# Kernel optimization log

Hardware: AMD Instinct MI355X
Metric: run time of the kernel (lower is better)

The kernel has to match this reference:

```python
import jax, jax.numpy as jnp
import numpy as np

B, S, D_MODEL, H, D = 2, 2048, 1024, 16, 64
SCALE = 1.0 / float(np.sqrt(D))


def setup_inputs() -> dict:
    key = jax.random.key(0)
    ks = jax.random.split(key, 5)
    x = jax.random.normal(ks[0], (B, S, D_MODEL), jnp.float32)
    qkv_w = jax.random.normal(ks[1], (3 * H * D, D_MODEL), jnp.float32) * 0.02
    out_w = jax.random.normal(ks[2], (D_MODEL, H * D), jnp.float32) * 0.02
    bias_p = jax.random.uniform(ks[3], (H, 1, 1), jnp.float32) * 2.0  # torch.rand(...)*2
    bias_a = jax.random.uniform(ks[4], (H, 1, 1), jnp.float32)
    # standard geometric RoPE frequencies over d_head//2 = 32 channels
    rope_freqs = 10000.0 ** (-jnp.arange(D // 2, dtype=jnp.float32) / (D // 2))
    return {"x": x, "qkv_w": qkv_w, "out_w": out_w,
            "bias_p": bias_p, "bias_a": bias_a, "rope_freqs": rope_freqs}


def _rope(t, c, s):
    # t: [B,H,S,d]; c,s: [1,1,S,d/2]. Split-half rotation as in apply_rope.
    d2 = t.shape[-1] // 2
    t1, t2 = t[..., :d2], t[..., d2:]
    return jnp.concatenate([t1 * c - t2 * s, t1 * s + t2 * c], axis=-1)


def reference(x, qkv_w, out_w, bias_p, bias_a, rope_freqs):
    Bb, Ss, _ = x.shape
    qkv = (x @ qkv_w.T).reshape(Bb, Ss, 3, H, D)
    q = qkv[:, :, 0].transpose(0, 2, 1, 3)  # [B,H,S,d]
    k = qkv[:, :, 1].transpose(0, 2, 1, 3)
    v = qkv[:, :, 2].transpose(0, 2, 1, 3)
    pos = jnp.arange(Ss, dtype=jnp.float32)
    ang = pos[:, None] * rope_freqs[None, :]                 # [S, d/2]
    c = jnp.cos(ang)[None, None]
    s = jnp.sin(ang)[None, None]
    q = _rope(q, c, s)
    k = _rope(k, c, s)
    scores = jnp.einsum('bhqd,bhkd->bhqk', q, k) * SCALE     # [B,H,S,S]
    p = jnp.maximum(bias_p, 0.01)                            # clamp(min=0.01)
    a = jnp.maximum(bias_a, 0.01)
    dist = jnp.abs(pos[None, :] - pos[:, None])              # [S,S]
    kb = -p * jnp.log1p(a * dist)                            # [H,S,S]
    attn = jax.nn.softmax(scores + kb[None], axis=-1)
    out = jnp.einsum('bhqk,bhkd->bhqd', attn, v)             # [B,H,S,d]
    out = out.transpose(0, 2, 1, 3).reshape(Bb, Ss, H * D)
    return out @ out_w.T
```

## Files before the change

kernel.cpp:

```cpp
#include <hip/hip_runtime.h>
#include <math.h>

#define BATCH  2
#define SEQ    2048
#define DMODEL 1024
#define NH     16
#define HD     64
#define NQKV   3072
#define ROWS   (BATCH*SEQ)
#define QSCALE 0.18033688f

typedef unsigned short u16;
typedef unsigned int   u32;
typedef __bf16 bf16x8 __attribute__((ext_vector_type(8)));
typedef float  f32x4  __attribute__((ext_vector_type(4)));

typedef const __attribute__((address_space(1))) void* gptr_t;
typedef __attribute__((address_space(3))) void* lptr_t;

__device__ __forceinline__ void gload16(lptr_t l, const void* g) {
    __builtin_amdgcn_global_load_lds((gptr_t)g, l, 16, 0, 0);
}

__device__ __forceinline__ u16 f2bf(float f) {
    unsigned int u = __float_as_uint(f);
    u += 0x7FFFu + ((u >> 16) & 1u);
    return (u16)(u >> 16);
}
__device__ __forceinline__ u32 pk2(float lo, float hi) {
#if __has_builtin(__builtin_amdgcn_cvt_pk_bf16_f32)
    typedef __bf16 bf16x2 __attribute__((ext_vector_type(2)));
    union { bf16x2 v; u32 u; } cv;
    cv.v = __builtin_amdgcn_cvt_pk_bf16_f32(lo, hi);
    return cv.u;
#else
    return (u32)f2bf(lo) | ((u32)f2bf(hi) << 16);
#endif
}
__device__ __forceinline__ float fexp2(float x) {
#if __has_builtin(__builtin_amdgcn_exp2f)
    return __builtin_amdgcn_exp2f(x);
#else
    return exp2f(x);
#endif
}

#define NBC ((ROWS*DMODEL + NQKV*DMODEL + DMODEL*DMODEL) / 1024)
__global__ void prep_kernel(const float* __restrict__ a,
                            const float* __restrict__ b,
                            const float* __restrict__ c,
                            u16* __restrict__ oa, u16* __restrict__ ob,
                            u16* __restrict__ oc,
                            const float* __restrict__ freqs, float* __restrict__ cs_tab,
                            const float* __restrict__ bias_p,
                            const float* __restrict__ bias_a,
                            float* __restrict__ wtab)
{
    const int na = ROWS*DMODEL, nb = NQKV*DMODEL;
    int blk = blockIdx.x;
    if (blk < NBC) {
        int i = (blk * 256 + threadIdx.x) * 4;
        const float* s; u16* d; int base;
        if (i < na)           { s = a; d = oa; base = i; }
        else if (i < na + nb) { s = b; d = ob; base = i - na; }
        else                  { s = c; d = oc; base = i - na - nb; }
        float4 v = *(const float4*)(s + base);
        u16 o[4] = { f2bf(v.x), f2bf(v.y), f2bf(v.z), f2bf(v.w) };
        *(uint2*)(d + base) = *(const uint2*)o;
    } else if (blk < NBC + 256) {
        int idx = (blk - NBC) * 256 + threadIdx.x;
        int s = idx >> 5, d = idx & 31;
        float sn, cs;
        sincosf((float)s * freqs[d], &sn, &cs);
        cs_tab[idx * 2]     = cs;
        cs_tab[idx * 2 + 1] = sn;
    } else {
        int idx = (blk - NBC - 256) * 256 + threadIdx.x;
        int h = idx >> 11;
        int d = idx & (SEQ - 1);
        float p = fmaxf(bias_p[h], 0.01f);
        float aa = fmaxf(bias_a[h], 0.01f);
        wtab[idx] = __expf(-p * log1pf(aa * (float)d));
    }
}

__global__ __launch_bounds__(256) void gemm_qkv(
    const u16* __restrict__ A, const u16* __restrict__ B,
    const float* __restrict__ cs_tab,
    u16* __restrict__ Qb, u16* __restrict__ Kb, u16* __restrict__ Vt)
{
    const int K = DMODEL;
    __shared__ __align__(16) u16 As[128][32];
    __shared__ __align__(16) u16 Bs[128][32];
    const int tid  = threadIdx.x;
    const int wave = tid >> 6, lane = tid & 63;
    const int quad = lane >> 4, l16 = lane & 15;
    const int wrow = (wave >> 1) * 64, wcol = (wave & 1) * 64;
    const int bm = blockIdx.x * 128, bn = blockIdx.y * 128;

    const int srow = lane >> 2;
    const int scol = ((lane & 3) ^ (srow & 3)) * 8;
    const int fsw = (quad ^ (l16 & 3)) * 8;

    f32x4 acc[4][4];
#pragma unroll
    for (int i = 0; i < 4; ++i)
#pragma unroll
        for (int j = 0; j < 4; ++j) acc[i][j] = (f32x4){0.f,0.f,0.f,0.f};

    const u16* Ag0 = A + (size_t)(bm + wave*32 + srow)      * K + scol;
    const u16* Ag1 = A + (size_t)(bm + wave*32 + 16 + srow) * K + scol;
    const u16* Bg0 = B + (size_t)(bn + wave*32 + srow)      * K + scol;
    const u16* Bg1 = B + (size_t)(bn + wave*32 + 16 + srow) * K + scol;

    for (int k0 = 0; k0 < K; k0 += 32) {
        __syncthreads();
        gload16((lptr_t)&As[wave*32][0],      Ag0 + k0);
        gload16((lptr_t)&As[wave*32 + 16][0], Ag1 + k0);
        gload16((lptr_t)&Bs[wave*32][0],      Bg0 + k0);
        gload16((lptr_t)&Bs[wave*32 + 16][0], Bg1 + k0);
        __syncthreads();
        bf16x8 af[4], bfr[4];
#pragma unroll
        for (int i = 0; i < 4; ++i)
            af[i] = *(const bf16x8*)&As[wrow + i*16 + l16][fsw];
#pragma unroll
        for (int j = 0; j < 4; ++j)
            bfr[j] = *(const bf16x8*)&Bs[wcol + j*16 + l16][fsw];
#pragma unroll
        for (int i = 0; i < 4; ++i)
#pragma unroll
            for (int j = 0; j < 4; ++j)
                acc[i][j] = __builtin_amdgcn_mfma_f32_16x16x32_bf16(af[i], bfr[j], acc[i][j], 0, 0, 0);
    }

    const int tcol = (bn + wcol) >> 6;
    const int t = tcol >> 4, h = tcol & 15;
    const int bq = bm >> 11;
    const int sb = (bm & (SEQ - 1)) + wrow;
    const size_t hb = (size_t)(bq * NH + h) * SEQ * HD;

    if (t == 2) {
#pragma unroll
        for (int i = 0; i < 4; ++i) {
            const int s = sb + i*16 + quad*4;
#pragma unroll
            for (int j = 0; j < 4; ++j) {
                const int d = j*16 + l16;
                uint2 pv = make_uint2(pk2(acc[i][j][0], acc[i][j][1]),
                                      pk2(acc[i][j][2], acc[i][j][3]));
                *(uint2*)&Vt[hb + (size_t)d * SEQ + s] = pv;
            }
        }
    } else {
        const float sc = (t == 0) ? QSCALE : 1.0f;
        u16* dstb = ((t == 0) ? Qb : Kb) + hb;
#pragma unroll
        for (int i = 0; i < 4; ++i) {
#pragma unroll
            for (int r = 0; r < 4; ++r) {
                const int s = sb + i*16 + quad*4 + r;
                const float2* ct = (const float2*)(cs_tab + ((size_t)s * 32 + l16) * 2);
                float2 cs0 = ct[0];
                float2 cs1 = ct[16];
                float a0 = acc[i][0][r], a1 = acc[i][1][r];
                float a2 = acc[i][2][r], a3 = acc[i][3][r];
                u16* dst = dstb + (size_t)s * HD;
                dst[l16]      = f2bf((a0*cs0.x - a2*cs0.y) * sc);
                dst[16 + l16] = f2bf((a1*cs1.x - a3*cs1.y) * sc);
                dst[32 + l16] = f2bf((a0*cs0.y + a2*cs0.x) * sc);
                dst[48 + l16] = f2bf((a1*cs1.y + a3*cs1.x) * sc);
            }
        }
    }
}

__global__ __launch_bounds__(256) void gemm_out(
    const u16* __restrict__ A, const u16* __restrict__ B,
    float* __restrict__ Cout, int M, int N, int K)
{
    __shared__ __align__(16) u16 As[128][32];
    __shared__ __align__(16) u16 Bs[64][32];
    const int tid  = threadIdx.x;
    const int wave = tid >> 6, lane = tid & 63;
    const int quad = lane >> 4, l16 = lane & 15;
    const int wrow = (wave >> 1) * 64, wcol = (wave & 1) * 32;
    const int bm = blockIdx.x * 128, bn = blockIdx.y * 64;

    const int srow = lane >> 2;
    const int scol = ((lane & 3) ^ (srow & 3)) * 8;
    const int fsw = (quad ^ (l16 & 3)) * 8;

    f32x4 acc[4][2];
#pragma unroll
    for (int i = 0; i < 4; ++i)
#pragma unroll
        for (int j = 0; j < 2; ++j) acc[i][j] = (f32x4){0.f,0.f,0.f,0.f};

    const u16* Ag0 = A + (size_t)(bm + wave*32 + srow)      * K + scol;
    const u16* Ag1 = A + (size_t)(bm + wave*32 + 16 + srow) * K + scol;
    const u16* Bg0 = B + (size_t)(bn + wave*16 + srow)      * K + scol;

    for (int k0 = 0; k0 < K; k0 += 32) {
        __syncthreads();
        gload16((lptr_t)&As[wave*32][0],      Ag0 + k0);
        gload16((lptr_t)&As[wave*32 + 16][0], Ag1 + k0);
        gload16((lptr_t)&Bs[wave*16][0],      Bg0 + k0);
        __syncthreads();
        bf16x8 af[4], bfr[2];
#pragma unroll
        for (int i = 0; i < 4; ++i)
            af[i] = *(const bf16x8*)&As[wrow + i*16 + l16][fsw];
#pragma unroll
        for (int j = 0; j < 2; ++j)
            bfr[j] = *(const bf16x8*)&Bs[wcol + j*16 + l16][fsw];
#pragma unroll
        for (int i = 0; i < 4; ++i)
#pragma unroll
            for (int j = 0; j < 2; ++j)
                acc[i][j] = __builtin_amdgcn_mfma_f32_16x16x32_bf16(af[i], bfr[j], acc[i][j], 0, 0, 0);
    }

#pragma unroll
    for (int i = 0; i < 4; ++i)
#pragma unroll
        for (int j = 0; j < 2; ++j) {
            int col = bn + wcol + j*16 + l16;
#pragma unroll
            for (int r = 0; r < 4; ++r) {
                int row = bm + wrow + i*16 + quad*4 + r;
                Cout[(size_t)row * N + col] = acc[i][j][r];
            }
        }
}

__global__ __launch_bounds__(256, 4) void attn_mfma(
    const u16* __restrict__ Qb, const u16* __restrict__ Kb,
    const u16* __restrict__ Vt, const float* __restrict__ wtab,
    u16* __restrict__ attn_bf)
{
    __shared__ __align__(16) u16 Ps[4*64*32];
    __shared__ __align__(16) u16 Vs[64*128];
    __shared__ u32 ws2[192];
    __shared__ float lred[4][64];
    __shared__ float linv[64];

    const int tid = threadIdx.x;
    const int wave = tid >> 6, lane = tid & 63;
    const int quad = lane >> 4, l16 = lane & 15;
    const int q0 = blockIdx.x * 64, h = blockIdx.y, b = blockIdx.z;

    const u16* Qh = Qb + (size_t)(b * NH + h) * SEQ * HD;
    const u16* Kh = Kb + (size_t)(b * NH + h) * SEQ * HD;
    const u16* Vh = Vt + (size_t)(b * NH + h) * HD * SEQ;
    const float* wh = wtab + h * SEQ;

    bf16x8 qf0[4], qf1[4];
#pragma unroll
    for (int qj = 0; qj < 4; ++qj) {
        const u16* qr = Qh + (size_t)(q0 + qj*16 + l16) * HD + quad * 8;
        qf0[qj] = *(const bf16x8*)qr;
        qf1[qj] = *(const bf16x8*)(qr + 32);
    }

    const u16* Kf0 = Kh + (size_t)(wave*32 + l16) * HD + quad * 8;

    const int vsrow = lane >> 4;
    const u16* Vst[4];
#pragma unroll
    for (int i = 0; i < 4; ++i) {
        int d = wave*16 + i*4 + vsrow;
        int vscol = ((lane & 15) ^ (d & 7)) * 8;
        Vst[i] = Vh + (size_t)d * SEQ + vscol;
    }

    const int psw  = ((l16 >> 1) & 3) << 3;
    const int mb0  = 127 + l16 - wave*32 - quad*4 - 3;

    float l_p[4] = {0.f, 0.f, 0.f, 0.f};
    f32x4 o[4];
#pragma unroll
    for (int j = 0; j < 4; ++j) o[j] = (f32x4){0.f,0.f,0.f,0.f};

    for (int kt = 0; kt < SEQ / 128; ++kt) {
        const int k0 = kt * 128;

        bf16x8 kf[2][2];
#pragma unroll
        for (int kg = 0; kg < 2; ++kg) {
            const u16* kp = Kf0 + (size_t)(k0 + kg*16) * HD;
            kf[kg][0] = *(const bf16x8*)kp;
            kf[kg][1] = *(const bf16x8*)(kp + 32);
        }

        __syncthreads();
#pragma unroll
        for (int i = 0; i < 4; ++i)
            gload16((lptr_t)&Vs[(wave*16 + i*4)*128], Vst[i] + k0);
        if (tid < 192) {
            int i0 = (q0 - k0 - 127) + tid;
            int a0 = i0 < 0 ? -i0 : i0;  if (a0 > SEQ-1) a0 = SEQ-1;
            int i1 = i0 + 1;
            int a1 = i1 < 0 ? -i1 : i1;  if (a1 > SEQ-1) a1 = SEQ-1;
            ws2[tid] = pk2(wh[a0], wh[a1]);
        }

        f32x4 z[2][4];
#pragma unroll
        for (int kg = 0; kg < 2; ++kg)
#pragma unroll
            for (int qj = 0; qj < 4; ++qj) {
                f32x4 zz = (f32x4){0.f,0.f,0.f,0.f};
                zz = __builtin_amdgcn_mfma_f32_16x16x32_bf16(kf[kg][0], qf0[qj], zz, 0, 0, 0);
                zz = __builtin_amdgcn_mfma_f32_16x16x32_bf16(kf[kg][1], qf1[qj], zz, 0, 0, 0);
                z[kg][qj] = zz;
            }
        __syncthreads();

#pragma unroll
        for (int kg = 0; kg < 2; ++kg) {
#pragma unroll
            for (int qj = 0; qj < 4; ++qj) {
                const int mbase = mb0 + qj*16 - kg*16;
                u32 pA = ws2[mbase], pB = ws2[mbase + 2];
                float w3 = __uint_as_float(pA << 16);
                float w2 = __uint_as_float(pA & 0xffff0000u);
                float w1 = __uint_as_float(pB << 16);
                float w0 = __uint_as_float(pB & 0xffff0000u);
                float e0 = fexp2(z[kg][qj][0]) * w0, e1 = fexp2(z[kg][qj][1]) * w1;
                float e2 = fexp2(z[kg][qj][2]) * w2, e3 = fexp2(z[kg][qj][3]) * w3;
                l_p[qj] += (e0 + e1) + (e2 + e3);
                *(uint2*)&Ps[wave*2048 + (qj*16 + l16)*32
                             + ((kg*16 + quad*4) ^ psw)] =
                    make_uint2(pk2(e0, e1), pk2(e2, e3));
            }
        }
        __syncthreads();

        bf16x8 pf[4];
#pragma unroll
        for (int m = 0; m < 4; ++m)
            pf[m] = *(const bf16x8*)&Ps[m*2048 + (wave*16 + l16)*32
                                        + ((quad*8) ^ psw)];
#pragma unroll
        for (int j = 0; j < 4; ++j) {
            const int vrow = (j*16 + l16) * 128;
            const int vsw = l16 & 7;
#pragma unroll
            for (int m = 0; m < 4; ++m) {
                bf16x8 vf = *(const bf16x8*)&Vs[vrow + (((m*4 + quad) ^ vsw) * 8)];
                o[j] = __builtin_amdgcn_mfma_f32_16x16x32_bf16(pf[m], vf, o[j], 0, 0, 0);
            }
        }
    }

#pragma unroll
    for (int qj = 0; qj < 4; ++qj) {
        float l = l_p[qj];
        l += __shfl_xor(l, 16);
        l += __shfl_xor(l, 32);
        if (quad == 0) lred[wave][qj*16 + l16] = l;
    }
    __syncthreads();
    if (tid < 64)
        linv[tid] = 1.0f / (lred[0][tid] + lred[1][tid] + lred[2][tid] + lred[3][tid]);
    __syncthreads();
#pragma unroll
    for (int r = 0; r < 4; ++r) {
        const int q = wave*16 + quad*4 + r;
        float inv = linv[q];
        u16* dst = attn_bf + (size_t)(b * SEQ + q0 + q) * DMODEL + h * HD;
#pragma unroll
        for (int j = 0; j < 4; ++j)
            dst[j*16 + l16] = f2bf(o[j][r] * inv);
    }
}

extern "C" void kernel_launch(void* const* d_in, const int* in_sizes, int n_in,
                              void* d_out, int out_size, void* d_ws, size_t ws_size,
                              hipStream_t stream)
{
    (void)in_sizes; (void)n_in; (void)out_size; (void)ws_size;
    const float* x      = (const float*)d_in[0];
    const float* qkv_w  = (const float*)d_in[1];
    const float* out_w  = (const float*)d_in[2];
    const float* bias_p = (const float*)d_in[3];
    const float* bias_a = (const float*)d_in[4];
    const float* freqs  = (const float*)d_in[5];
    float* out = (float*)d_out;

    char* ws = (char*)d_ws;
    u16*   attn_bf = (u16*)ws;
    u16*   Qb      = (u16*)(ws + 8388608);
    u16*   x_bf    = (u16*)(ws + 25165824);
    u16*   w1_bf   = (u16*)(ws + 33554432);
    u16*   w2_bf   = (u16*)(ws + 39845888);
    u16*   Kb      = (u16*)(ws + 41943040);
    u16*   Vt      = (u16*)(ws + 50331648);
    float* wtab    = (float*)(ws + 58720256);
    float* cs_tab  = (float*)(ws + 58720256 + 131072);

    prep_kernel<<<dim3(NBC + 256 + 128), 256, 0, stream>>>(
        x, qkv_w, out_w, x_bf, w1_bf, w2_bf, freqs, cs_tab, bias_p, bias_a, wtab);

    gemm_qkv<<<dim3(ROWS/128, NQKV/128), 256, 0, stream>>>(x_bf, w1_bf, cs_tab, Qb, Kb, Vt);
    attn_mfma<<<dim3(SEQ/64, NH, BATCH), 256, 0, stream>>>(Qb, Kb, Vt, wtab, attn_bf);
    gemm_out<<<dim3(ROWS/128, DMODEL/64), 256, 0, stream>>>(attn_bf, w2_bf, out, ROWS, DMODEL, DMODEL);
}
```

Baseline: 221.9 us.

## Load V fragments directly from global and double-buffer bias table in attention loop

The attention kernel no longer stages the V tile in shared memory. Each wave reads its V fragments straight from global memory, which can be L2-cached. The distance-bias table is double-buffered, and the next tile's entries are prefetched at the end of each iteration, cutting barriers per tile from three to two and fusing the QK MFMA with the exp/weighting step. In exchange, every wave re-reads the same V data from global or cache instead of sharing one LDS copy, which can raise memory traffic and latency.

```diff
diff --git a/kernel.cpp b/kernel.cpp
--- a/kernel.cpp
+++ b/kernel.cpp
@@ -240,8 +240,7 @@
     u16* __restrict__ attn_bf)
 {
     __shared__ __align__(16) u16 Ps[4*64*32];
-    __shared__ __align__(16) u16 Vs[64*128];
-    __shared__ u32 ws2[192];
+    __shared__ u32 ws2[2][192];
     __shared__ float lred[4][64];
     __shared__ float linv[64];
 
@@ -265,14 +264,10 @@
 
     const u16* Kf0 = Kh + (size_t)(wave*32 + l16) * HD + quad * 8;
 
-    const int vsrow = lane >> 4;
-    const u16* Vst[4];
-#pragma unroll
-    for (int i = 0; i < 4; ++i) {
-        int d = wave*16 + i*4 + vsrow;
-        int vscol = ((lane & 15) ^ (d & 7)) * 8;
-        Vst[i] = Vh + (size_t)d * SEQ + vscol;
-    }
+    const u16* Vrow[4];
+#pragma unroll
+    for (int j = 0; j < 4; ++j)
+        Vrow[j] = Vh + (size_t)(j*16 + l16) * SEQ + quad * 8;
 
     const int psw  = ((l16 >> 1) & 3) << 3;
     const int mb0  = 127 + l16 - wave*32 - quad*4 - 3;
@@ -282,8 +277,18 @@
 #pragma unroll
     for (int j = 0; j < 4; ++j) o[j] = (f32x4){0.f,0.f,0.f,0.f};
 
+    if (tid < 192) {
+        int i0 = (q0 - 127) + tid;
+        int a0 = i0 < 0 ? -i0 : i0;  if (a0 > SEQ-1) a0 = SEQ-1;
+        int i1 = i0 + 1;
+        int a1 = i1 < 0 ? -i1 : i1;  if (a1 > SEQ-1) a1 = SEQ-1;
+        ws2[0][tid] = pk2(wh[a0], wh[a1]);
+    }
+    __syncthreads();
+
     for (int kt = 0; kt < SEQ / 128; ++kt) {
         const int k0 = kt * 128;
+        const u32* wsb = ws2[kt & 1];
 
         bf16x8 kf[2][2];
 #pragma unroll
@@ -293,42 +298,21 @@
             kf[kg][1] = *(const bf16x8*)(kp + 32);
         }
 
-        __syncthreads();
-#pragma unroll
-        for (int i = 0; i < 4; ++i)
-            gload16((lptr_t)&Vs[(wave*16 + i*4)*128], Vst[i] + k0);
-        if (tid < 192) {
-            int i0 = (q0 - k0 - 127) + tid;
-            int a0 = i0 < 0 ? -i0 : i0;  if (a0 > SEQ-1) a0 = SEQ-1;
-            int i1 = i0 + 1;
-            int a1 = i1 < 0 ? -i1 : i1;  if (a1 > SEQ-1) a1 = SEQ-1;
-            ws2[tid] = pk2(wh[a0], wh[a1]);
-        }
-
-        f32x4 z[2][4];
-#pragma unroll
-        for (int kg = 0; kg < 2; ++kg)
+#pragma unroll
+        for (int kg = 0; kg < 2; ++kg) {
 #pragma unroll
             for (int qj = 0; qj < 4; ++qj) {
                 f32x4 zz = (f32x4){0.f,0.f,0.f,0.f};
                 zz = __builtin_amdgcn_mfma_f32_16x16x32_bf16(kf[kg][0], qf0[qj], zz, 0, 0, 0);
                 zz = __builtin_amdgcn_mfma_f32_16x16x32_bf16(kf[kg][1], qf1[qj], zz, 0, 0, 0);
-                z[kg][qj] = zz;
-            }
-        __syncthreads();
-
-#pragma unroll
-        for (int kg = 0; kg < 2; ++kg) {
-#pragma unroll
-            for (int qj = 0; qj < 4; ++qj) {
                 const int mbase = mb0 + qj*16 - kg*16;
-                u32 pA = ws2[mbase], pB = ws2[mbase + 2];
+                u32 pA = wsb[mbase], pB = wsb[mbase + 2];
                 float w3 = __uint_as_float(pA << 16);
                 float w2 = __uint_as_float(pA & 0xffff0000u);
                 float w1 = __uint_as_float(pB << 16);
                 float w0 = __uint_as_float(pB & 0xffff0000u);
-                float e0 = fexp2(z[kg][qj][0]) * w0, e1 = fexp2(z[kg][qj][1]) * w1;
-                float e2 = fexp2(z[kg][qj][2]) * w2, e3 = fexp2(z[kg][qj][3]) * w3;
+                float e0 = fexp2(zz[0]) * w0, e1 = fexp2(zz[1]) * w1;
+                float e2 = fexp2(zz[2]) * w2, e3 = fexp2(zz[3]) * w3;
                 l_p[qj] += (e0 + e1) + (e2 + e3);
                 *(uint2*)&Ps[wave*2048 + (qj*16 + l16)*32
                              + ((kg*16 + quad*4) ^ psw)] =
@@ -344,14 +328,22 @@
                                         + ((quad*8) ^ psw)];
 #pragma unroll
         for (int j = 0; j < 4; ++j) {
-            const int vrow = (j*16 + l16) * 128;
-            const int vsw = l16 & 7;
+            const u16* vb = Vrow[j] + k0;
 #pragma unroll
             for (int m = 0; m < 4; ++m) {
-                bf16x8 vf = *(const bf16x8*)&Vs[vrow + (((m*4 + quad) ^ vsw) * 8)];
+                bf16x8 vf = *(const bf16x8*)(vb + m*32);
                 o[j] = __builtin_amdgcn_mfma_f32_16x16x32_bf16(pf[m], vf, o[j], 0, 0, 0);
             }
         }
+
+        if (kt + 1 < SEQ / 128 && tid < 192) {
+            int i0 = (q0 - (kt+1)*128 - 127) + tid;
+            int a0 = i0 < 0 ? -i0 : i0;  if (a0 > SEQ-1) a0 = SEQ-1;
+            int i1 = i0 + 1;
+            int a1 = i1 < 0 ? -i1 : i1;  if (a1 > SEQ-1) a1 = SEQ-1;
+            ws2[(kt+1) & 1][tid] = pk2(wh[a0], wh[a1]);
+        }
+        __syncthreads();
     }
 
 #pragma unroll
```

Result: slower. 305.2 us (+37.6%).
